# Kernel optimization log

Hardware: AMD Instinct MI355X
Metric: run time of the kernel (lower is better)

## Reference

```python
import jax, jax.numpy as jnp
import numpy as np

N = 4096          # n_nodes
M = 8192          # m_nodes (= 2*N, required by block structure)
D = 128           # in_dim == hidden_dim (conv1 is reapplied to its own output)
H = 128
NUM_ITERS = 3


def setup_inputs() -> dict:
    key = jax.random.key(0)
    ks = jax.random.split(key, 6)
    X = jax.random.normal(ks[0], (N, D), dtype=jnp.float32)
    R = jax.random.uniform(ks[1], (N, N), dtype=jnp.float32)
    A = 0.5 * (R + R.T)  # symmetric, strictly positive connectivity matrix
    # upsample MLP: Linear(n_nodes -> m_nodes - n_nodes), torch weight layout [out, in]
    W_up = jax.random.normal(ks[2], (M - N, N), dtype=jnp.float32) * 0.02
    b_up = jnp.zeros((M - N,), dtype=jnp.float32)
    # GCNConv linear weights stored [in, out]
    W1 = jax.random.normal(ks[3], (D, H), dtype=jnp.float32) * 0.05
    b1 = jnp.zeros((H,), dtype=jnp.float32)
    W2 = jax.random.normal(ks[4], (H, H), dtype=jnp.float32) * 0.05
    b2 = jnp.zeros((H,), dtype=jnp.float32)
    return dict(X=X, A=A, W_up=W_up, b_up=b_up, W1=W1, b1=b1, W2=W2, b2=b2)


def _gcn(Adj, X, W, b):
    # PyG GCNConv on a fully dense, strictly-positive weighted graph:
    # every diagonal entry is nonzero, so add_remaining_self_loops is a no-op and
    # out = D^{-1/2} A D^{-1/2} (X W) + b  exactly.
    deg = Adj.sum(axis=0)                         # [m] column degree
    dinv = jnp.where(deg > 0, jax.lax.rsqrt(deg), 0.0)
    An = Adj * dinv[:, None] * dinv[None, :]      # symmetric normalization
    return An @ (X @ W) + b


def reference(X, A, W_up, b_up, W1, b1, W2, b2):
    # new_nodes = upsample_mlp(X.T).T  -> [M-N, D]
    new_nodes = (X.T @ W_up.T + b_up).T
    Xu = jnp.concatenate([X, new_nodes], axis=0)  # [M, D]
    # block adjacency: [[A, A.T], [A, sigmoid(new @ new.T)]]
    Adj = jnp.block([[A, A.T],
                     [A, jax.nn.sigmoid(new_nodes @ new_nodes.T)]])  # [M, M]
    A_out = Adj
    for _ in range(NUM_ITERS):
        Xu = jax.nn.relu(_gcn(Adj, Xu, W1, b1))
        Adj = jax.nn.sigmoid(Xu @ Xu.T)           # mid-loop adjacency rebuild
        Xu = jax.nn.relu(_gcn(Adj, Xu, W2, b2))
        A_out = jax.nn.sigmoid(Xu @ Xu.T)
        # NOTE: edge_index for the next conv1 is NOT rebuilt from A_out in the
        # original (only after conv1), so Adj carries the mid-loop matrix.
    return A_out
```

## Files before the change

kernel.cpp:

```cpp
#include <hip/hip_runtime.h>
#include <hip/hip_bf16.h>


#define N_NODES 4096
#define M_NODES 8192
#define DIM 128
#define SLICE_ELEMS ((size_t)M_NODES * DIM)

typedef __attribute__((ext_vector_type(4))) float f32x4;
typedef __attribute__((ext_vector_type(8))) short bf16x8;
typedef __attribute__((ext_vector_type(8))) _Float16 half8;

__device__ __forceinline__ unsigned short f2bf(float f) {
  union { float f; unsigned u; } v; v.f = f;
  unsigned r = v.u + 0x7fffu + ((v.u >> 16) & 1u);
  return (unsigned short)(r >> 16);
}

__device__ __forceinline__ unsigned short f2h(float f) {
  union { _Float16 h; unsigned short u; } v; v.h = (_Float16)f; return v.u;
}

__device__ __forceinline__ unsigned char f2e5(float f) {
  unsigned short h = f2h(f);
  unsigned short r = h + 0x7Fu + ((h >> 8) & 1u);
  return (unsigned char)(r >> 8);
}
__device__ __forceinline__ float e5tof(unsigned char b) {
  union { unsigned short u; _Float16 h; } v; v.u = (unsigned short)b << 8;
  return (float)v.h;
}

__device__ __forceinline__ void gld16(unsigned short* lds, const unsigned short* g) {
  __builtin_amdgcn_global_load_lds(
      (const __attribute__((address_space(1))) unsigned int*)g,
      (__attribute__((address_space(3))) unsigned int*)lds, 16, 0, 0);
}
__device__ __forceinline__ void gld16b(unsigned char* lds, const unsigned char* g) {
  __builtin_amdgcn_global_load_lds(
      (const __attribute__((address_space(1))) unsigned int*)g,
      (__attribute__((address_space(3))) unsigned int*)lds, 16, 0, 0);
}

__device__ __forceinline__ float sigmoidf_(float x) { return 1.0f / (1.0f + __expf(-x)); }

__device__ __forceinline__ half8 expandA(const unsigned char* la, int row, int c16, int hf) {
  const unsigned* p =
      (const unsigned*)&la[(((c16 ^ (row & 3)) * 64 + row) * 16) + hf * 8];
  unsigned x0 = p[0], x1 = p[1];
  union { unsigned u[4]; half8 h; } r;
  r.u[0] = __builtin_amdgcn_perm(x0, 0u, 0x050C040Cu);
  r.u[1] = __builtin_amdgcn_perm(x0, 0u, 0x070C060Cu);
  r.u[2] = __builtin_amdgcn_perm(x1, 0u, 0x050C040Cu);
  r.u[3] = __builtin_amdgcn_perm(x1, 0u, 0x070C060Cu);
  return r.h;
}


__global__ void cast_x_kernel(const float* __restrict__ X, unsigned short* __restrict__ Xu,
                              unsigned short* __restrict__ XT,
                              const float* __restrict__ W1, const float* __restrict__ W2,
                              unsigned short* __restrict__ W1T,
                              unsigned short* __restrict__ W2T,
                              float* __restrict__ deg) {
  int idx = blockIdx.x * 256 + threadIdx.x;
  if (idx < M_NODES) deg[idx] = 0.f;
  if (idx < 32768) {
    const float* W = idx < 16384 ? W1 : W2;
    unsigned short* WT = idx < 16384 ? W1T : W2T;
    int j = idx & 16383;
    int k = j >> 7, c = j & 127;
    WT[c * DIM + k] = f2bf(W[j]);
  }
  int i = idx >> 7, c = idx & 127;
  unsigned short b = f2bf(X[idx]);
  Xu[idx] = b;
  XT[(size_t)c * N_NODES + i] = b;
}

__global__ void cast_a_kernel(const float* __restrict__ A, unsigned char* __restrict__ Adj,
                              float* __restrict__ deg) {
  int c = blockIdx.x * 256 + threadIdx.x;
  int r0 = blockIdx.y * 128;
  int tm = r0 >> 7;
  int kc = c >> 10, st = (c & 1023) >> 5, e = c & 31;
  size_t a1 = ((size_t)(tm)      * 8 + kc)     * 131072 + (size_t)st * 4096 + e;
  size_t a2 = ((size_t)(tm)      * 8 + 4 + kc) * 131072 + (size_t)st * 4096 + e;
  size_t a3 = ((size_t)(tm + 32) * 8 + kc)     * 131072 + (size_t)st * 4096 + e;
  float s = 0.f;
  for (int r = 0; r < 128; ++r) {
    float a = A[(size_t)(r0 + r) * N_NODES + c];
    unsigned char b = f2e5(a);
    Adj[a1 + r * 32] = b; Adj[a2 + r * 32] = b; Adj[a3 + r * 32] = b;
    s += e5tof(b);
  }
  atomicAdd(&deg[c], 2.0f * s);
  atomicAdd(&deg[N_NODES + c], s);
}


__global__ __launch_bounds__(256, 2)
void aggf8_kernel(const unsigned char* __restrict__ At,
                  const unsigned short* __restrict__ BT, long ldb,
                  float* __restrict__ accBase) {
  __shared__ __align__(16) unsigned char smem[61440];
  const int t = threadIdx.x, w = t >> 6, lane = t & 63;
  const int q = lane >> 4, l15 = lane & 15;
  const int wm = w & 1, wn = w >> 1;
  const int tm = blockIdx.x >> 1;
  const int hrow = (blockIdx.x & 1) * 64;
  const int sg0 = blockIdx.y * 64;
  const int arow = lane;
  const int ac16 = w ^ (lane & 3);

  auto STAGE = [&](int s, int b) {
    unsigned char* la = smem + b * 20480;
    unsigned short* lb = (unsigned short*)(la + 4096);
    int sg = sg0 + 2 * s + (ac16 >> 1);
    gld16b(&la[t * 16],
           &At[((size_t)tm * 8 + (sg >> 5)) * 131072 + (size_t)(sg & 31) * 4096 +
               (hrow + arow) * 32 + (ac16 & 1) * 16]);
    size_t kb = (size_t)sg0 * 32 + (size_t)s * 64;
#pragma unroll
    for (int j = 0; j < 4; ++j) {
      int ch = j * 256 + t;
      int row = ch >> 3, phys = ch & 7;
      int c = phys ^ (row & 7);
      gld16(&lb[ch * 8], &BT[(size_t)row * ldb + kb + c * 8]);
    }
  };

  f32x4 acc[2][4];
#pragma unroll
  for (int a = 0; a < 2; ++a)
#pragma unroll
    for (int b = 0; b < 4; ++b) acc[a][b] = (f32x4)0.f;

  STAGE(0, 0);
  STAGE(1, 1);

  for (int s = 0; s < 32; ++s) {
    if (s + 2 < 32) {
      STAGE(s + 2, (s + 2) % 3);
      asm volatile("s_waitcnt vmcnt(10)" ::: "memory");
    } else if (s + 1 < 32) {
      asm volatile("s_waitcnt vmcnt(5)" ::: "memory");
    } else {
      asm volatile("s_waitcnt vmcnt(0)" ::: "memory");
    }
    __builtin_amdgcn_s_barrier();
    __builtin_amdgcn_sched_barrier(0);

    const unsigned char* la = smem + (s % 3) * 20480;
    const unsigned short* lb = (const unsigned short*)(la + 4096);
#pragma unroll
    for (int kk = 0; kk < 2; ++kk) {
      int ch8 = kk * 4 + q;
      int c16 = ch8 >> 1, hf = ch8 & 1;
      half8 a0 = expandA(la, wm * 32 + l15, c16, hf);
      half8 a1 = expandA(la, wm * 32 + 16 + l15, c16, hf);
#pragma unroll
      for (int nt = 0; nt < 4; ++nt) {
        int brow = wn * 64 + nt * 16 + l15;
        half8 b = *(const half8*)&lb[brow * 64 + (ch8 ^ (l15 & 7)) * 8];
        acc[0][nt] = __builtin_amdgcn_mfma_f32_16x16x32_f16(a0, b, acc[0][nt], 0, 0, 0);
        acc[1][nt] = __builtin_amdgcn_mfma_f32_16x16x32_f16(a1, b, acc[1][nt], 0, 0, 0);
      }
    }
    __builtin_amdgcn_sched_barrier(0);
    __builtin_amdgcn_s_barrier();
    __builtin_amdgcn_sched_barrier(0);
  }
  float* ct = accBase + (size_t)blockIdx.y * SLICE_ELEMS + (size_t)blockIdx.x * 8192;
#pragma unroll
  for (int mt = 0; mt < 2; ++mt)
#pragma unroll
    for (int nt = 0; nt < 4; ++nt)
      *(f32x4*)&ct[((w * 8 + mt * 4 + nt) * 256) + (q * 16 + l15) * 4] = acc[mt][nt];
}


__global__ __launch_bounds__(256)
void up_agg_f32(const float* __restrict__ Wup, const unsigned short* __restrict__ BT,
                float* __restrict__ accBase) {
  __shared__ __align__(16) unsigned short smem[6144];
  unsigned short* la = smem;
  unsigned short* lb = smem + 2048;
  const int t = threadIdx.x, w = t >> 6, lane = t & 63;
  const int q = lane >> 4, l15 = lane & 15;
  const int r0 = blockIdx.x * 64;
  const int k0 = blockIdx.y * 512;
  const int arow = t >> 2, achk = t & 3;

  f32x4 acc[8];
#pragma unroll
  for (int b = 0; b < 8; ++b) acc[b] = (f32x4)0.f;

  for (int s = 0; s < 16; ++s) {
    int kb = k0 + s * 32;
    __syncthreads();
    gld16(&lb[t * 8],        &BT[(size_t)arow * N_NODES + kb + achk * 8]);
    gld16(&lb[2048 + t * 8], &BT[(size_t)(64 + arow) * N_NODES + kb + achk * 8]);
    const float* ap = &Wup[(size_t)(r0 + (t >> 2)) * N_NODES + kb + (t & 3) * 8];
    float4 v0 = *(const float4*)ap;
    float4 v1 = *(const float4*)(ap + 4);
    ushort4 o0, o1;
    o0.x = f2bf(v0.x); o0.y = f2bf(v0.y); o0.z = f2bf(v0.z); o0.w = f2bf(v0.w);
    o1.x = f2bf(v1.x); o1.y = f2bf(v1.y); o1.z = f2bf(v1.z); o1.w = f2bf(v1.w);
    *(ushort4*)&la[t * 8] = o0;
    *(ushort4*)&la[t * 8 + 4] = o1;
    __syncthreads();

    bf16x8 a0 = *(const bf16x8*)&la[(w * 16 + l15) * 32 + q * 8];
#pragma unroll
    for (int nt = 0; nt < 8; ++nt) {
      bf16x8 b = *(const bf16x8*)&lb[(nt * 16 + l15) * 32 + q * 8];
      acc[nt] = __builtin_amdgcn_mfma_f32_16x16x32_bf16(a0, b, acc[nt], 0, 0, 0);
    }
  }
  float* ct = accBase + (size_t)blockIdx.y * SLICE_ELEMS + (size_t)blockIdx.x * 8192;
#pragma unroll
  for (int nt = 0; nt < 8; ++nt)
    *(f32x4*)&ct[((w * 8 + nt) * 256) + (q * 16 + l15) * 4] = acc[nt];
}

__global__ void reduce64_kernel(const float* __restrict__ acc,
                                unsigned short* __restrict__ dst,
                                const float* __restrict__ bias_row,
                                const float* __restrict__ bias_col,
                                const float* __restrict__ deg, int mode, int nSlices) {
  int p = blockIdx.x * 256 + threadIdx.x;
  float s = 0.f;
  for (int sp = 0; sp < nSlices; ++sp) s += acc[(size_t)sp * SLICE_ELEMS + p];
  int tile = p >> 13, r = p & 8191;
  int grp = r >> 8;
  int r2 = r & 255;
  int i = r2 & 3, ql = r2 >> 2;
  int row, col;
  float v;
  if (mode == 0) {
    int w = grp >> 3, nt = grp & 7;
    row = tile * 64 + w * 16 + (ql >> 4) * 4 + i;
    col = nt * 16 + (ql & 15);
    v = s + bias_row[row];
  } else {
    int w = grp >> 3, mt = (grp >> 2) & 1, nt = grp & 3;
    row = tile * 64 + (w & 1) * 32 + mt * 16 + (ql >> 4) * 4 + i;
    col = (w >> 1) * 64 + nt * 16 + (ql & 15);
    float d = deg[row];
    float dv = d > 0.f ? rsqrtf(d) : 0.f;
    v = fmaxf(dv * s + bias_col[col], 0.f);
  }
  dst[(size_t)row * DIM + col] = f2bf(v);
}


template <int MODE>
__global__ __launch_bounds__(256)
void rebuild_kernel(const unsigned short* __restrict__ XA,
                    const unsigned short* __restrict__ XB,
                    void* __restrict__ out, long p1 ,
                    long col0, float* __restrict__ deg, int nB) {
  __shared__ __align__(16) unsigned short smem[34816];
  __shared__ float lcol[128];
  __shared__ float lrow[128];
  unsigned short* lA = smem;
  unsigned short* lB = smem + 16384;
  const int t = threadIdx.x, w = t >> 6, lane = t & 63;
  const int q = lane >> 4, l15 = lane & 15;
  const int sx = (l15 >> 1) & 3;

  int rem = blockIdx.x, bi = 0;
  while (rem >= nB - bi) { rem -= nB - bi; ++bi; }
  const int bj = bi + rem;
  const int i0 = bi * 128, j0 = bj * 128;
  const bool offdiag = (bi != bj);

  const int srow = t >> 2;
  const int xchk = (t & 3) ^ ((t >> 3) & 3);
#pragma unroll
  for (int kk = 0; kk < 4; ++kk)
#pragma unroll
    for (int h = 0; h < 2; ++h) {
      gld16(&lA[kk * 4096 + h * 2048 + t * 8],
            &XA[(size_t)(i0 + h * 64 + srow) * DIM + kk * 32 + xchk * 8]);
      gld16(&lB[kk * 4096 + h * 2048 + t * 8],
            &XB[(size_t)(j0 + h * 64 + srow) * DIM + kk * 32 + xchk * 8]);
    }
  if (MODE == 0 && t < 128) { lcol[t] = 0.f; lrow[t] = 0.f; }
  __syncthreads();

  f32x4 acc[2][8];
#pragma unroll
  for (int a = 0; a < 2; ++a)
#pragma unroll
    for (int b = 0; b < 8; ++b) acc[a][b] = (f32x4)0.f;

#pragma unroll
  for (int kk = 0; kk < 4; ++kk) {
    bf16x8 a0 = *(const bf16x8*)&lA[kk * 4096 + (w * 32 + l15) * 32 + ((q ^ sx)) * 8];
    bf16x8 a1 = *(const bf16x8*)&lA[kk * 4096 + (w * 32 + 16 + l15) * 32 + ((q ^ sx)) * 8];
#pragma unroll
    for (int nt = 0; nt < 8; ++nt) {
      bf16x8 b = *(const bf16x8*)&lB[kk * 4096 + (nt * 16 + l15) * 32 + ((q ^ sx)) * 8];
      acc[0][nt] = __builtin_amdgcn_mfma_f32_16x16x32_bf16(a0, b, acc[0][nt], 0, 0, 0);
      acc[1][nt] = __builtin_amdgcn_mfma_f32_16x16x32_bf16(a1, b, acc[1][nt], 0, 0, 0);
    }
  }
  __syncthreads();

  if (MODE == 0) {
    unsigned char* lC  = (unsigned char*)smem;
    unsigned char* lCt = (unsigned char*)smem + 17408;
    float rs[2][4] = {{0.f, 0.f, 0.f, 0.f}, {0.f, 0.f, 0.f, 0.f}};
#pragma unroll
    for (int mt = 0; mt < 2; ++mt)
#pragma unroll
      for (int nt = 0; nt < 8; ++nt) {
        float cs = 0.f;
#pragma unroll
        for (int i = 0; i < 4; ++i) {
          unsigned char hb = f2e5(sigmoidf_(acc[mt][nt][i]));
          float dq = e5tof(hb);
          cs += dq;
          int row = w * 32 + mt * 16 + q * 4 + i, colL = nt * 16 + l15;
          lC[row * 136 + colL] = hb;
          if (offdiag) { lCt[colL * 136 + row] = hb; rs[mt][i] += dq; }
        }
        cs += __shfl_xor(cs, 16);
        cs += __shfl_xor(cs, 32);
        if (lane < 16) atomicAdd(&lcol[nt * 16 + lane], cs);
      }
    if (offdiag) {
#pragma unroll
      for (int mt = 0; mt < 2; ++mt)
#pragma unroll
        for (int i = 0; i < 4; ++i) {
          float v = rs[mt][i];
          v += __shfl_xor(v, 1); v += __shfl_xor(v, 2);
          v += __shfl_xor(v, 4); v += __shfl_xor(v, 8);
          if (l15 == 0) atomicAdd(&lrow[w * 32 + mt * 16 + q * 4 + i], v);
        }
    }
    __syncthreads();
    unsigned char* og = (unsigned char*)out;
    {
      const long rowbase = p1 + i0, colbase = col0 + j0;
      const size_t tb = ((size_t)(rowbase >> 7) * 8 + (colbase >> 10)) * 131072;
      const int stb = (int)((colbase & 1023) >> 5);
#pragma unroll
      for (int cc = 0; cc < 8; ++cc) {
        int ch = t + cc * 256;
        int row = ch >> 4, c16 = ch & 15;
        *(unsigned long long*)
            &og[tb + (size_t)(stb + (c16 >> 2)) * 4096 + row * 32 + (c16 & 3) * 8] =
            *(const unsigned long long*)&lC[row * 136 + c16 * 8];
      }
    }
    if (offdiag) {
      const long rowbase = p1 + j0, colbase = col0 + i0;
      const size_t tb = ((size_t)(rowbase >> 7) * 8 + (colbase >> 10)) * 131072;
      const int stb = (int)((colbase & 1023) >> 5);
#pragma unroll
      for (int cc = 0; cc < 8; ++cc) {
        int ch = t + cc * 256;
        int row = ch >> 4, c16 = ch & 15;
        *(unsigned long long*)
            &og[tb + (size_t)(stb + (c16 >> 2)) * 4096 + row * 32 + (c16 & 3) * 8] =
            *(const unsigned long long*)&lCt[row * 136 + c16 * 8];
      }
    }
    if (t < 128) atomicAdd(&deg[col0 + j0 + t], lcol[t]);
    if (offdiag && t < 128) atomicAdd(&deg[col0 + i0 + t], lrow[t]);
  } else {
    float* og = (float*)out;
    float* lCf = (float*)smem;
#pragma unroll
    for (int mt = 0; mt < 2; ++mt)
#pragma unroll
      for (int nt = 0; nt < 8; ++nt)
#pragma unroll
        for (int i = 0; i < 4; ++i) acc[mt][nt][i] = sigmoidf_(acc[mt][nt][i]);
#pragma unroll
    for (int h2 = 0; h2 < 2; ++h2) {
      __syncthreads();
      if ((w >> 1) == h2) {
#pragma unroll
        for (int mt = 0; mt < 2; ++mt)
#pragma unroll
          for (int nt = 0; nt < 8; ++nt)
#pragma unroll
            for (int i = 0; i < 4; ++i)
              lCf[((w & 1) * 32 + mt * 16 + q * 4 + i) * 132 + nt * 16 + l15] =
                  acc[mt][nt][i];
      }
      __syncthreads();
#pragma unroll
      for (int j = 0; j < 8; ++j) {
        int ch = t + j * 256;
        int r64 = ch >> 5, c4 = (ch & 31) * 4;
        *(f32x4*)&og[(size_t)(i0 + h2 * 64 + r64) * p1 + j0 + c4] =
            *(const f32x4*)&lCf[r64 * 132 + c4];
      }
    }
    if (offdiag) {
#pragma unroll
      for (int h2 = 0; h2 < 2; ++h2) {
        __syncthreads();
#pragma unroll
        for (int mt = 0; mt < 2; ++mt)
#pragma unroll
          for (int nt = 0; nt < 8; ++nt)
            if ((nt >> 2) == h2) {
#pragma unroll
              for (int i = 0; i < 4; ++i)
                lCf[((nt & 3) * 16 + l15) * 132 + (w * 32 + mt * 16 + q * 4 + i)] =
                    acc[mt][nt][i];
            }
        __syncthreads();
#pragma unroll
        for (int j = 0; j < 8; ++j) {
          int ch = t + j * 256;
          int r64 = ch >> 5, c4 = (ch & 31) * 4;
          *(f32x4*)&og[(size_t)(j0 + h2 * 64 + r64) * p1 + i0 + c4] =
              *(const f32x4*)&lCf[r64 * 132 + c4];
        }
      }
    }
  }
}


__global__ __launch_bounds__(256)
void yz_kernel(const unsigned short* __restrict__ Xu, const unsigned short* __restrict__ WT,
               const float* __restrict__ deg, unsigned short* __restrict__ ZT, int ldz,
               float* __restrict__ zbuf) {
  __shared__ __align__(16) unsigned short smem[32768];
  unsigned short* lA = smem;
  unsigned short* lB = smem + 16384;
  const int t = threadIdx.x, w = t >> 6, lane = t & 63;
  const int q = lane >> 4, l15 = lane & 15;
  const int sx = (l15 >> 1) & 3;
  const int r0 = blockIdx.x * 128;
  if (zbuf) {
    int gid = blockIdx.x * 256 + t;
    if (gid < M_NODES) zbuf[gid] = 0.f;
  }
  const int srow = t >> 2;
  const int xchk = (t & 3) ^ ((t >> 3) & 3);
#pragma unroll
  for (int kk = 0; kk < 4; ++kk)
#pragma unroll
    for (int h = 0; h < 2; ++h) {
      gld16(&lA[kk * 4096 + h * 2048 + t * 8],
            &Xu[(size_t)(r0 + h * 64 + srow) * DIM + kk * 32 + xchk * 8]);
      gld16(&lB[kk * 4096 + h * 2048 + t * 8],
            &WT[(size_t)(h * 64 + srow) * DIM + kk * 32 + xchk * 8]);
    }
  __syncthreads();

  f32x4 acc[2][8];
#pragma unroll
  for (int a = 0; a < 2; ++a)
#pragma unroll
    for (int b = 0; b < 8; ++b) acc[a][b] = (f32x4)0.f;

#pragma unroll
  for (int kk = 0; kk < 4; ++kk) {
    bf16x8 a0 = *(const bf16x8*)&lA[kk * 4096 + (w * 32 + l15) * 32 + (q ^ sx) * 8];
    bf16x8 a1 = *(const bf16x8*)&lA[kk * 4096 + (w * 32 + 16 + l15) * 32 + (q ^ sx) * 8];
#pragma unroll
    for (int nt = 0; nt < 8; ++nt) {
      bf16x8 b = *(const bf16x8*)&lB[kk * 4096 + (nt * 16 + l15) * 32 + (q ^ sx) * 8];
      acc[0][nt] = __builtin_amdgcn_mfma_f32_16x16x32_bf16(a0, b, acc[0][nt], 0, 0, 0);
      acc[1][nt] = __builtin_amdgcn_mfma_f32_16x16x32_bf16(a1, b, acc[1][nt], 0, 0, 0);
    }
  }
  __syncthreads();
  unsigned short* lT = smem;
#pragma unroll
  for (int mt = 0; mt < 2; ++mt)
#pragma unroll
    for (int i = 0; i < 4; ++i) {
      int r = w * 32 + mt * 16 + q * 4 + i;
      float d = deg[r0 + r];
      float dv = d > 0.f ? rsqrtf(d) : 0.f;
#pragma unroll
      for (int nt = 0; nt < 8; ++nt)
        lT[(nt * 16 + l15) * 136 + r] = f2h(dv * acc[mt][nt][i]);
    }
  __syncthreads();
#pragma unroll
  for (int cc = 0; cc < 8; ++cc) {
    int ch = t + cc * 256;
    int c = ch >> 4, c16 = ch & 15;
    *(bf16x8*)&ZT[(size_t)c * ldz + r0 + c16 * 8] = *(const bf16x8*)&lT[c * 136 + c16 * 8];
  }
}


extern "C" void kernel_launch(void* const* d_in, const int* in_sizes, int n_in,
                              void* d_out, int out_size, void* d_ws, size_t ws_size,
                              hipStream_t stream) {
  (void)in_sizes; (void)n_in; (void)out_size;
  const float* X   = (const float*)d_in[0];
  const float* A   = (const float*)d_in[1];
  const float* Wup = (const float*)d_in[2];
  const float* bup = (const float*)d_in[3];
  const float* W1  = (const float*)d_in[4];
  const float* b1  = (const float*)d_in[5];
  const float* W2  = (const float*)d_in[6];
  const float* b2  = (const float*)d_in[7];

  const size_t ADJ_BYTES = (size_t)M_NODES * M_NODES;
  char* ws = (char*)d_ws;
  size_t off = 0;
  auto alloc = [&](size_t bytes) {
    char* p = ws + off;
    off += (bytes + 255) & ~(size_t)255;
    return p;
  };
  float*          accb    = (float*)alloc(8 * SLICE_ELEMS * 4);
  unsigned short* Xu      = (unsigned short*)alloc((size_t)M_NODES * DIM * 2);
  unsigned short* ZT      = (unsigned short*)alloc((size_t)DIM * M_NODES * 2);
  unsigned short* XT      = (unsigned short*)alloc((size_t)DIM * N_NODES * 2);
  unsigned short* W1T     = (unsigned short*)alloc(DIM * DIM * 2);
  unsigned short* W2T     = (unsigned short*)alloc(DIM * DIM * 2);
  float*          degA    = (float*)alloc(M_NODES * 4);
  float*          degB    = (float*)alloc(M_NODES * 4);

  unsigned char* Adj;
  if (ws_size >= off + ADJ_BYTES) Adj = (unsigned char*)(ws + off);
  else                            Adj = (unsigned char*)d_out;

  unsigned short* XuNew = Xu + (size_t)N_NODES * DIM;

  cast_x_kernel<<<N_NODES * DIM / 256, 256, 0, stream>>>(X, Xu, XT, W1, W2, W1T, W2T, degA);

  up_agg_f32<<<dim3(N_NODES / 64, 8), 256, 0, stream>>>(Wup, XT, accb);
  reduce64_kernel<<<N_NODES * DIM / 256, 256, 0, stream>>>(
      accb, XuNew, bup, nullptr, nullptr, 0, 8);

  cast_a_kernel<<<dim3(N_NODES / 256, N_NODES / 128), 256, 0, stream>>>(A, Adj, degA);
  rebuild_kernel<0><<<32 * 33 / 2, 256, 0, stream>>>(
      XuNew, XuNew, Adj, N_NODES, N_NODES, degA, 32);

  float* degCur = degA;
  float* degMid = degB;
  for (int it = 0; it < 3; ++it) {
    yz_kernel<<<M_NODES / 128, 256, 0, stream>>>(Xu, W1T, degCur, ZT, M_NODES, degMid);
    aggf8_kernel<<<dim3(M_NODES / 64, 4), 256, 0, stream>>>(Adj, ZT, M_NODES, accb);
    reduce64_kernel<<<M_NODES * DIM / 256, 256, 0, stream>>>(
        accb, Xu, nullptr, b1, degCur, 1, 4);
    rebuild_kernel<0><<<64 * 65 / 2, 256, 0, stream>>>(
        Xu, Xu, Adj, 0, 0, degMid, 64);
    yz_kernel<<<M_NODES / 128, 256, 0, stream>>>(Xu, W2T, degMid, ZT, M_NODES, nullptr);
    aggf8_kernel<<<dim3(M_NODES / 64, 4), 256, 0, stream>>>(Adj, ZT, M_NODES, accb);
    reduce64_kernel<<<M_NODES * DIM / 256, 256, 0, stream>>>(
        accb, Xu, nullptr, b2, degMid, 1, 4);
    if (it == 2)
      rebuild_kernel<1><<<64 * 65 / 2, 256, 0, stream>>>(
          Xu, Xu, d_out, M_NODES, 0, nullptr, 64);
    float* tmp = degCur; degCur = degMid; degMid = tmp;
  }
}
```

Baseline: 834.1 us.

## Replace split-K aggregation plus reduce with full-K 16-row tiles and fused epilogue

The adjacency-times-features aggregation kernel no longer splits K four ways into fp32 partial slices that a separate reduce kernel sums. Each block now covers 16 rows over the full K range and applies degree normalization, bias, ReLU and the bf16 cast in its own epilogue, so one launch and the slice write/read traffic disappear. In exchange, per-block tiles are much smaller (16x128 instead of 64x128), so each block reloads the full ZT operand. That raises B-side L2 traffic and lowers MFMA work per loaded byte. The loop is also four times longer per block.

```diff
diff --git a/kernel.cpp b/kernel.cpp
--- a/kernel.cpp
+++ b/kernel.cpp
@@ -44,9 +44,8 @@
 
 __device__ __forceinline__ float sigmoidf_(float x) { return 1.0f / (1.0f + __expf(-x)); }
 
-__device__ __forceinline__ half8 expandA(const unsigned char* la, int row, int c16, int hf) {
-  const unsigned* p =
-      (const unsigned*)&la[(((c16 ^ (row & 3)) * 64 + row) * 16) + hf * 8];
+__device__ __forceinline__ half8 expand8(const unsigned char* p8) {
+  const unsigned* p = (const unsigned*)p8;
   unsigned x0 = p[0], x1 = p[1];
   union { unsigned u[4]; half8 h; } r;
   r.u[0] = __builtin_amdgcn_perm(x0, 0u, 0x050C040Cu);
@@ -100,27 +99,25 @@
 
 
 __global__ __launch_bounds__(256, 2)
-void aggf8_kernel(const unsigned char* __restrict__ At,
-                  const unsigned short* __restrict__ BT, long ldb,
-                  float* __restrict__ accBase) {
-  __shared__ __align__(16) unsigned char smem[61440];
+void aggf8_16(const unsigned char* __restrict__ At,
+              const unsigned short* __restrict__ BT, long ldb,
+              unsigned short* __restrict__ Xout,
+              const float* __restrict__ bias_col, const float* __restrict__ deg) {
+  __shared__ __align__(16) unsigned char smem[52224];
   const int t = threadIdx.x, w = t >> 6, lane = t & 63;
   const int q = lane >> 4, l15 = lane & 15;
-  const int wm = w & 1, wn = w >> 1;
-  const int tm = blockIdx.x >> 1;
-  const int hrow = (blockIdx.x & 1) * 64;
-  const int sg0 = blockIdx.y * 64;
-  const int arow = lane;
-  const int ac16 = w ^ (lane & 3);
+  const int tm = blockIdx.x >> 3;
+  const int rb = (blockIdx.x & 7) * 16;
+  const int arow = lane & 15, ac16 = lane >> 4;
 
   auto STAGE = [&](int s, int b) {
-    unsigned char* la = smem + b * 20480;
-    unsigned short* lb = (unsigned short*)(la + 4096);
-    int sg = sg0 + 2 * s + (ac16 >> 1);
-    gld16b(&la[t * 16],
+    unsigned char* la = smem + b * 17408;
+    unsigned short* lb = (unsigned short*)(la + 1024);
+    int sg = 2 * s + (ac16 >> 1);
+    gld16b(&la[lane * 16],
            &At[((size_t)tm * 8 + (sg >> 5)) * 131072 + (size_t)(sg & 31) * 4096 +
-               (hrow + arow) * 32 + (ac16 & 1) * 16]);
-    size_t kb = (size_t)sg0 * 32 + (size_t)s * 64;
+               (rb + arow) * 32 + (ac16 & 1) * 16]);
+    size_t kb = (size_t)s * 64;
 #pragma unroll
     for (int j = 0; j < 4; ++j) {
       int ch = j * 256 + t;
@@ -130,20 +127,17 @@
     }
   };
 
-  f32x4 acc[2][4];
-#pragma unroll
-  for (int a = 0; a < 2; ++a)
-#pragma unroll
-    for (int b = 0; b < 4; ++b) acc[a][b] = (f32x4)0.f;
+  f32x4 acc[2];
+  acc[0] = (f32x4)0.f; acc[1] = (f32x4)0.f;
 
   STAGE(0, 0);
   STAGE(1, 1);
 
-  for (int s = 0; s < 32; ++s) {
-    if (s + 2 < 32) {
+  for (int s = 0; s < 128; ++s) {
+    if (s + 2 < 128) {
       STAGE(s + 2, (s + 2) % 3);
       asm volatile("s_waitcnt vmcnt(10)" ::: "memory");
-    } else if (s + 1 < 32) {
+    } else if (s + 1 < 128) {
       asm volatile("s_waitcnt vmcnt(5)" ::: "memory");
     } else {
       asm volatile("s_waitcnt vmcnt(0)" ::: "memory");
@@ -151,32 +145,36 @@
     __builtin_amdgcn_s_barrier();
     __builtin_amdgcn_sched_barrier(0);
 
-    const unsigned char* la = smem + (s % 3) * 20480;
-    const unsigned short* lb = (const unsigned short*)(la + 4096);
+    const unsigned char* la = smem + (s % 3) * 17408;
+    const unsigned short* lb = (const unsigned short*)(la + 1024);
 #pragma unroll
     for (int kk = 0; kk < 2; ++kk) {
       int ch8 = kk * 4 + q;
       int c16 = ch8 >> 1, hf = ch8 & 1;
-      half8 a0 = expandA(la, wm * 32 + l15, c16, hf);
-      half8 a1 = expandA(la, wm * 32 + 16 + l15, c16, hf);
-#pragma unroll
-      for (int nt = 0; nt < 4; ++nt) {
-        int brow = wn * 64 + nt * 16 + l15;
+      half8 a0 = expand8(&la[(c16 * 16 + l15) * 16 + hf * 8]);
+#pragma unroll
+      for (int nt = 0; nt < 2; ++nt) {
+        int brow = w * 32 + nt * 16 + l15;
         half8 b = *(const half8*)&lb[brow * 64 + (ch8 ^ (l15 & 7)) * 8];
-        acc[0][nt] = __builtin_amdgcn_mfma_f32_16x16x32_f16(a0, b, acc[0][nt], 0, 0, 0);
-        acc[1][nt] = __builtin_amdgcn_mfma_f32_16x16x32_f16(a1, b, acc[1][nt], 0, 0, 0);
+        acc[nt] = __builtin_amdgcn_mfma_f32_16x16x32_f16(a0, b, acc[nt], 0, 0, 0);
       }
     }
     __builtin_amdgcn_sched_barrier(0);
     __builtin_amdgcn_s_barrier();
     __builtin_amdgcn_sched_barrier(0);
   }
-  float* ct = accBase + (size_t)blockIdx.y * SLICE_ELEMS + (size_t)blockIdx.x * 8192;
-#pragma unroll
-  for (int mt = 0; mt < 2; ++mt)
-#pragma unroll
-    for (int nt = 0; nt < 4; ++nt)
-      *(f32x4*)&ct[((w * 8 + mt * 4 + nt) * 256) + (q * 16 + l15) * 4] = acc[mt][nt];
+
+#pragma unroll
+  for (int i = 0; i < 4; ++i) {
+    int row = blockIdx.x * 16 + q * 4 + i;
+    float d = deg[row];
+    float dv = d > 0.f ? rsqrtf(d) : 0.f;
+#pragma unroll
+    for (int nt = 0; nt < 2; ++nt) {
+      int col = w * 32 + nt * 16 + l15;
+      Xout[(size_t)row * DIM + col] = f2bf(fmaxf(dv * acc[nt][i] + bias_col[col], 0.f));
+    }
+  }
 }
 
 
@@ -226,32 +224,18 @@
 
 __global__ void reduce64_kernel(const float* __restrict__ acc,
                                 unsigned short* __restrict__ dst,
-                                const float* __restrict__ bias_row,
-                                const float* __restrict__ bias_col,
-                                const float* __restrict__ deg, int mode, int nSlices) {
+                                const float* __restrict__ bias_row, int nSlices) {
   int p = blockIdx.x * 256 + threadIdx.x;
   float s = 0.f;
   for (int sp = 0; sp < nSlices; ++sp) s += acc[(size_t)sp * SLICE_ELEMS + p];
   int tile = p >> 13, r = p & 8191;
   int grp = r >> 8;
+  int w = grp >> 3, nt = grp & 7;
   int r2 = r & 255;
   int i = r2 & 3, ql = r2 >> 2;
-  int row, col;
-  float v;
-  if (mode == 0) {
-    int w = grp >> 3, nt = grp & 7;
-    row = tile * 64 + w * 16 + (ql >> 4) * 4 + i;
-    col = nt * 16 + (ql & 15);
-    v = s + bias_row[row];
-  } else {
-    int w = grp >> 3, mt = (grp >> 2) & 1, nt = grp & 3;
-    row = tile * 64 + (w & 1) * 32 + mt * 16 + (ql >> 4) * 4 + i;
-    col = (w >> 1) * 64 + nt * 16 + (ql & 15);
-    float d = deg[row];
-    float dv = d > 0.f ? rsqrtf(d) : 0.f;
-    v = fmaxf(dv * s + bias_col[col], 0.f);
-  }
-  dst[(size_t)row * DIM + col] = f2bf(v);
+  int row = tile * 64 + w * 16 + (ql >> 4) * 4 + i;
+  int col = nt * 16 + (ql & 15);
+  dst[(size_t)row * DIM + col] = f2bf(s + bias_row[row]);
 }
 
 
@@ -538,8 +522,7 @@
   cast_x_kernel<<<N_NODES * DIM / 256, 256, 0, stream>>>(X, Xu, XT, W1, W2, W1T, W2T, degA);
 
   up_agg_f32<<<dim3(N_NODES / 64, 8), 256, 0, stream>>>(Wup, XT, accb);
-  reduce64_kernel<<<N_NODES * DIM / 256, 256, 0, stream>>>(
-      accb, XuNew, bup, nullptr, nullptr, 0, 8);
+  reduce64_kernel<<<N_NODES * DIM / 256, 256, 0, stream>>>(accb, XuNew, bup, 8);
 
   cast_a_kernel<<<dim3(N_NODES / 256, N_NODES / 128), 256, 0, stream>>>(A, Adj, degA);
   rebuild_kernel<0><<<32 * 33 / 2, 256, 0, stream>>>(
@@ -549,15 +532,11 @@
   float* degMid = degB;
   for (int it = 0; it < 3; ++it) {
     yz_kernel<<<M_NODES / 128, 256, 0, stream>>>(Xu, W1T, degCur, ZT, M_NODES, degMid);
-    aggf8_kernel<<<dim3(M_NODES / 64, 4), 256, 0, stream>>>(Adj, ZT, M_NODES, accb);
-    reduce64_kernel<<<M_NODES * DIM / 256, 256, 0, stream>>>(
-        accb, Xu, nullptr, b1, degCur, 1, 4);
+    aggf8_16<<<M_NODES / 16, 256, 0, stream>>>(Adj, ZT, M_NODES, Xu, b1, degCur);
     rebuild_kernel<0><<<64 * 65 / 2, 256, 0, stream>>>(
         Xu, Xu, Adj, 0, 0, degMid, 64);
     yz_kernel<<<M_NODES / 128, 256, 0, stream>>>(Xu, W2T, degMid, ZT, M_NODES, nullptr);
-    aggf8_kernel<<<dim3(M_NODES / 64, 4), 256, 0, stream>>>(Adj, ZT, M_NODES, accb);
-    reduce64_kernel<<<M_NODES * DIM / 256, 256, 0, stream>>>(
-        accb, Xu, nullptr, b2, degMid, 1, 4);
+    aggf8_16<<<M_NODES / 16, 256, 0, stream>>>(Adj, ZT, M_NODES, Xu, b2, degMid);
     if (it == 2)
       rebuild_kernel<1><<<64 * 65 / 2, 256, 0, stream>>>(
           Xu, Xu, d_out, M_NODES, 0, nullptr, 64);
```

Result: slower. 1.000 ms (+19.9%).
